# Kernel optimization log

Measured on AMD Instinct MI355X. Metric: run time of the kernel, lower is better.

Reference implementation:

```python
import jax, jax.numpy as jnp
import numpy as np

B, D_IN, H, D_OUT = 256, 512, 512, 10
S = 32          # num posterior samples
MAXITER = 10    # fixed CG steps (solve_normaleq_cg_fixed_step_reortho(maxiter=10))
EPS = 1e-12


def mlp(params, x):
    W1, b1, W2, b2 = params
    h = jnp.tanh(x @ W1 + b1)
    return h @ W2 + b2  # [B, D_OUT]


def setup_inputs() -> dict:
    key = jax.random.key(0)
    ks = jax.random.split(key, 8)
    s = lambda k, shape, scale=1.0: jax.random.normal(k, shape, dtype=jnp.float32) * scale
    return {
        "x": s(ks[0], (B, D_IN)),
        "W1": s(ks[1], (D_IN, H), 1.0 / np.sqrt(D_IN)),
        "b1": jnp.zeros((H,), jnp.float32),
        "W2": s(ks[2], (H, D_OUT), 1.0 / np.sqrt(H)),
        "b2": jnp.zeros((D_OUT,), jnp.float32),
        "eps_W1": s(ks[3], (S, D_IN, H)),
        "eps_b1": s(ks[4], (S, H)),
        "eps_W2": s(ks[5], (S, H, D_OUT)),
        "eps_b2": s(ks[6], (S, D_OUT)),
        "log_precision": jnp.zeros((), jnp.float32),
        "log_scale_image": jnp.asarray(-2.0, jnp.float32),
    }


def _posterior_predict(x, W1, b1, W2, b2, eps_W1, eps_b1, eps_W2, eps_b2,
                       log_precision, log_scale_image):
    params = (W1, b1, W2, b2)
    f = lambda p: mlp(p, x)
    out0, jvp_lin = jax.linearize(f, params)  # out0: [B, D_OUT]
    _, vjp_fn = jax.vjp(f, params)
    N = B * D_OUT

    def matvec(u_flat):  # u: [N] -> (J J^T) u : [N]
        (t,) = vjp_fn(u_flat.reshape(B, D_OUT))  # J^T u (param pytree)
        return jvp_lin(t).ravel()                # J J^T u

    def cg_reortho(b):  # fixed-step CG with full reorthogonalization
        rn0 = jnp.linalg.norm(b)
        basis0 = jnp.zeros((MAXITER + 1, N), b.dtype).at[0].set(b / (rn0 + EPS))

        def step(carry, k):
            a, r, p, basis = carry
            Ap = matvec(p)
            rr = jnp.vdot(r, r)
            alpha = rr / (jnp.vdot(p, Ap) + EPS)
            a = a + alpha * p
            r_new = r - alpha * Ap
            # Gram-Schmidt reorthogonalization against stored residual basis
            r_new = r_new - basis.T @ (basis @ r_new)
            beta = jnp.vdot(r_new, r_new) / (rr + EPS)
            p = r_new + beta * p
            basis = basis.at[k + 1].set(r_new / (jnp.linalg.norm(r_new) + EPS))
            return (a, r_new, p, basis), jnp.linalg.norm(r_new)

        init = (jnp.zeros_like(b), b, b, basis0)
        (a, _, _, _), resnorms = jax.lax.scan(step, init, jnp.arange(MAXITER))
        return a, resnorms

    def kernel_projection(eps):  # eps: param-pytree iso noise sample
        b = jvp_lin(eps).ravel()          # J v
        a, resnorms = cg_reortho(b)       # (J J^T)^{-1} J v
        (kv,) = vjp_fn(a.reshape(B, D_OUT))  # kernel component J^T a
        return kv, resnorms

    iso = (eps_W1, eps_b1, eps_W2, eps_b2)  # leading axis S
    kernel, resnorms = jax.vmap(kernel_projection)(iso)
    image = jax.tree_util.tree_map(lambda i, k: i - k, iso, kernel)

    # linearized output sampling: f(mean) + J @ (s_k * kernel + s_i * image)
    sk = jnp.exp(-0.5 * log_precision)  # log_scale_kernel = -0.5 * log_precision
    si = jnp.exp(log_scale_image)
    perturb = jax.tree_util.tree_map(lambda kv, iv: sk * kv + si * iv, kernel, image)
    preds = out0[None] + jax.vmap(jvp_lin)(perturb)  # [S, B, D_OUT]
    return preds


def reference(x, W1, b1, W2, b2, eps_W1, eps_b1, eps_W2, eps_b2,
              log_precision, log_scale_image):
    return _posterior_predict(x, W1, b1, W2, b2, eps_W1, eps_b1, eps_W2,
                              eps_b2, log_precision, log_scale_image)
```

## Files before the change

kernel.cpp:

```cpp
#include <hip/hip_runtime.h>
#include <math.h>

#define BB    256
#define DIN   512
#define HD    512
#define DOUT  10
#define NS    32
#define NIDX  2560
#define MAXIT 10
#define CG_EPS 1e-12f

typedef __attribute__((ext_vector_type(8))) short s16x8;
typedef __attribute__((ext_vector_type(4))) float f32x4;

__device__ __forceinline__ float wave_red(float v){
  #pragma unroll
  for (int off = 32; off > 0; off >>= 1) v += __shfl_down(v, off, 64);
  return v;
}
__device__ __forceinline__ unsigned short f2bf(float f){
  unsigned u = __float_as_uint(f);
  return (unsigned short)((u + 0x7FFFu + ((u >> 16) & 1u)) >> 16);
}
__device__ __forceinline__ float bf2f(unsigned short h){
  return __uint_as_float((unsigned)h << 16);
}

typedef const __attribute__((address_space(1))) unsigned short gus_t;
typedef __attribute__((address_space(3))) unsigned short lus_t;
__device__ __forceinline__ void gload16(const unsigned short* g, unsigned short* l){
  __builtin_amdgcn_global_load_lds((gus_t*)g, (lus_t*)l, 16, 0, 0);
}

__global__ __launch_bounds__(256) void k_gemm_z(
    const float* __restrict__ x, const float* __restrict__ W1,
    const float* __restrict__ b1, float* __restrict__ h, float* __restrict__ G)
{
  __shared__ __align__(16) float Al[16][68];
  __shared__ __align__(16) float Bl[16][64];
  const int tid = threadIdx.x;
  const int m0 = blockIdx.y * 64, n0 = blockIdx.x * 64;
  const int tx = tid & 15, ty = tid >> 4;
  float acc[4][4] = {};
  for (int k0 = 0; k0 < DIN; k0 += 16){
    {
      int m = tid >> 2, kk = (tid & 3) << 2;
      float4 a = *(const float4*)(x + (size_t)(m0+m)*DIN + k0 + kk);
      Al[kk+0][m]=a.x; Al[kk+1][m]=a.y; Al[kk+2][m]=a.z; Al[kk+3][m]=a.w;
    }
    {
      int kk = tid >> 4, n = (tid & 15) << 2;
      *(float4*)&Bl[kk][n] = *(const float4*)(W1 + (size_t)(k0+kk)*HD + n0 + n);
    }
    __syncthreads();
    #pragma unroll
    for (int kk = 0; kk < 16; kk++){
      float4 av = *(const float4*)&Al[kk][ty<<2];
      float4 bv = *(const float4*)&Bl[kk][tx<<2];
      float aa[4]={av.x,av.y,av.z,av.w}, bb[4]={bv.x,bv.y,bv.z,bv.w};
      #pragma unroll
      for (int i=0;i<4;i++)
        #pragma unroll
        for (int j=0;j<4;j++) acc[i][j] += aa[i]*bb[j];
    }
    __syncthreads();
  }
  float4 b4 = *(const float4*)&b1[n0 + (tx<<2)];
  float bbv[4] = {b4.x,b4.y,b4.z,b4.w};
  #pragma unroll
  for (int i=0;i<4;i++){
    int m = m0 + (ty<<2) + i;
    float hh[4], gg[4];
    #pragma unroll
    for (int j=0;j<4;j++){ float t = tanhf(acc[i][j] + bbv[j]); hh[j]=t; gg[j]=1.0f-t*t; }
    *(float4*)&h[(size_t)m*HD + n0 + (tx<<2)] = make_float4(hh[0],hh[1],hh[2],hh[3]);
    *(float4*)&G[(size_t)m*HD + n0 + (tx<<2)] = make_float4(gg[0],gg[1],gg[2],gg[3]);
  }
}

__global__ __launch_bounds__(256) void k_gemm_kxkh(
    const float* __restrict__ x, const float* __restrict__ h,
    float* __restrict__ Kx, float* __restrict__ Kh)
{
  __shared__ __align__(16) float Al[16][68];
  __shared__ __align__(16) float Bl[16][68];
  const int tid = threadIdx.x;
  const float* A = blockIdx.z ? h : x;
  float* C = blockIdx.z ? Kh : Kx;
  const int m0 = blockIdx.y * 64, n0 = blockIdx.x * 64;
  const int tx = tid & 15, ty = tid >> 4;
  float acc[4][4] = {};
  for (int k0 = 0; k0 < DIN; k0 += 16){
    {
      int m = tid >> 2, kk = (tid & 3) << 2;
      float4 a = *(const float4*)(A + (size_t)(m0+m)*DIN + k0 + kk);
      Al[kk+0][m]=a.x; Al[kk+1][m]=a.y; Al[kk+2][m]=a.z; Al[kk+3][m]=a.w;
      float4 b = *(const float4*)(A + (size_t)(n0+m)*DIN + k0 + kk);
      Bl[kk+0][m]=b.x; Bl[kk+1][m]=b.y; Bl[kk+2][m]=b.z; Bl[kk+3][m]=b.w;
    }
    __syncthreads();
    #pragma unroll
    for (int kk = 0; kk < 16; kk++){
      float4 av = *(const float4*)&Al[kk][ty<<2];
      float4 bv = *(const float4*)&Bl[kk][tx<<2];
      float aa[4]={av.x,av.y,av.z,av.w}, bb[4]={bv.x,bv.y,bv.z,bv.w};
      #pragma unroll
      for (int i=0;i<4;i++)
        #pragma unroll
        for (int j=0;j<4;j++) acc[i][j] += aa[i]*bb[j];
    }
    __syncthreads();
  }
  #pragma unroll
  for (int i=0;i<4;i++){
    int m = m0 + (ty<<2) + i;
    *(float4*)&C[(size_t)m*BB + n0 + (tx<<2)] =
        make_float4(acc[i][0]+1.0f, acc[i][1]+1.0f, acc[i][2]+1.0f, acc[i][3]+1.0f);
  }
}

__global__ __launch_bounds__(256) void k_buildE(
    const float* __restrict__ G, const float* __restrict__ W2,
    unsigned short* __restrict__ E2)
{
  int gid = blockIdx.x * 256 + threadIdx.x;
  int row = gid >> 7, j4 = (gid & 127) << 2;
  int b = row / 10, o = row - b * 10;
  float4 g = *(const float4*)&G[(size_t)b*HD + j4];
  float e[4] = { g.x * W2[(j4+0)*DOUT + o], g.y * W2[(j4+1)*DOUT + o],
                 g.z * W2[(j4+2)*DOUT + o], g.w * W2[(j4+3)*DOUT + o] };
  unsigned short hi[4], lo[4];
  #pragma unroll
  for (int r = 0; r < 4; r++){
    hi[r] = f2bf(e[r]);
    lo[r] = f2bf(e[r] - bf2f(hi[r]));
  }
  *(ushort4*)&E2[(size_t)row*1024 + j4]       = make_ushort4(hi[0],hi[1],hi[2],hi[3]);
  *(ushort4*)&E2[(size_t)row*1024 + 512 + j4] = make_ushort4(lo[0],lo[1],lo[2],lo[3]);
}

__global__ __launch_bounds__(256) void k_prepx(
    const float* __restrict__ x, unsigned short* __restrict__ x2)
{
  int gid = blockIdx.x * 256 + threadIdx.x;
  int row = gid >> 7, j4 = (gid & 127) << 2;
  float4 v = *(const float4*)&x[(size_t)row*DIN + j4];
  float e[4] = {v.x, v.y, v.z, v.w};
  unsigned short hi[4], lo[4];
  #pragma unroll
  for (int r = 0; r < 4; r++){
    hi[r] = f2bf(e[r]);
    lo[r] = f2bf(e[r] - bf2f(hi[r]));
  }
  *(ushort4*)&x2[(size_t)row*1024 + j4]       = make_ushort4(hi[0],hi[1],hi[2],hi[3]);
  *(ushort4*)&x2[(size_t)row*1024 + 512 + j4] = make_ushort4(lo[0],lo[1],lo[2],lo[3]);
}

__global__ __launch_bounds__(128) void k_gemm_M(
    const unsigned short* __restrict__ E2, const float* __restrict__ Kx,
    const float* __restrict__ Kh, unsigned short* __restrict__ M2)
{
  __shared__ __align__(16) unsigned short As[128*64];
  __shared__ __align__(16) unsigned short Bs[64*64];
  const int tid = threadIdx.x;
  const int w = tid >> 6, l = tid & 63;
  const int ln = l & 15, kq = l >> 4;
  const int orig = blockIdx.x;
  const int wg = (orig & 7) * 100 + (orig >> 3);
  const int m0 = (wg / 40) << 7, n0 = (wg % 40) << 6;

  const int srow = tid >> 3;
  const int scc  = (tid & 7) ^ (srow & 7);
  const unsigned short* gA = E2 + (size_t)(m0 + srow)*1024 + scc*8;
  const unsigned short* gB = E2 + (size_t)(n0 + srow)*1024 + scc*8;
  unsigned short* lA = As + ((tid & 64) << 3);
  unsigned short* lB = Bs + ((tid & 64) << 3);

  f32x4 acc[4][4];
  #pragma unroll
  for (int i = 0; i < 4; i++)
    #pragma unroll
    for (int j = 0; j < 4; j++)
      acc[i][j] = (f32x4){0.f, 0.f, 0.f, 0.f};

  const int xs = ln & 7;

  for (int t = 0; t < 24; ++t){
    const int p = t >> 3, k8 = t & 7;
    const int oa = ((p == 2) ? 512 : 0) + (k8 << 6);
    const int ob = ((p == 1) ? 512 : 0) + (k8 << 6);
    #pragma unroll
    for (int c = 0; c < 8; c++)
      gload16(gA + (size_t)c*16*1024 + oa, lA + c*1024);
    #pragma unroll
    for (int c = 0; c < 4; c++)
      gload16(gB + (size_t)c*16*1024 + ob, lB + c*1024);
    __syncthreads();

    #pragma unroll
    for (int kk = 0; kk < 2; kk++){
      const int kc = kq + (kk << 2);
      const int co = (kc ^ xs) << 3;
      s16x8 af[4], bf[4];
      #pragma unroll
      for (int f = 0; f < 4; f++){
        af[f] = *(const s16x8*)(As + ((w<<6) + (f<<4) + ln)*64 + co);
        bf[f] = *(const s16x8*)(Bs + ((f<<4) + ln)*64 + co);
      }
      #pragma unroll
      for (int fi = 0; fi < 4; fi++)
        #pragma unroll
        for (int fj = 0; fj < 4; fj++)
          acc[fi][fj] = __builtin_amdgcn_mfma_f32_16x16x32_bf16(
              af[fi], bf[fj], acc[fi][fj], 0, 0, 0);
    }
    __syncthreads();
  }

  const int mb = m0 + (w << 6);
  int bmv[4][4], omv[4][4], bnv[4], onv[4];
  #pragma unroll
  for (int f = 0; f < 4; f++){
    int n = n0 + f*16 + ln; bnv[f] = n / 10; onv[f] = n - bnv[f]*10;
    #pragma unroll
    for (int r = 0; r < 4; r++){
      int m = mb + f*16 + kq*4 + r;
      bmv[f][r] = m / 10; omv[f][r] = m - bmv[f][r]*10;
    }
  }
  #pragma unroll
  for (int fi = 0; fi < 4; fi++)
    #pragma unroll
    for (int r = 0; r < 4; r++){
      const int m = mb + fi*16 + kq*4 + r;
      #pragma unroll
      for (int fj = 0; fj < 4; fj++){
        const int n = n0 + fj*16 + ln;
        float v = Kx[(size_t)bmv[fi][r]*BB + bnv[fj]] * acc[fi][fj][r];
        if (omv[fi][r] == onv[fj]) v += Kh[(size_t)bmv[fi][r]*BB + bnv[fj]];
        unsigned short hv = f2bf(v);
        M2[(size_t)m*5120 + n]        = hv;
        M2[(size_t)m*5120 + 2560 + n] = f2bf(v - bf2f(hv));
      }
    }
}

__global__ __launch_bounds__(512) void k_gemm_T(
    const unsigned short* __restrict__ x2, const float* __restrict__ eW1,
    const float* __restrict__ eb1, const float* __restrict__ G,
    float* __restrict__ T)
{
  const int tid = threadIdx.x;
  const int w = tid >> 6, l = tid & 63;
  const int ln = l & 15, kq = l >> 4;
  const int n0 = blockIdx.x << 6;
  const int s  = blockIdx.y;
  const float* Wb = eW1 + (size_t)s * DIN * HD;

  const unsigned short* pa[2];
  #pragma unroll
  for (int f = 0; f < 2; f++)
    pa[f] = x2 + (size_t)(16*(2*w + f) + ln) * 1024 + kq * 8;

  f32x4 acc[2][4];
  #pragma unroll
  for (int i = 0; i < 2; i++)
    #pragma unroll
    for (int j = 0; j < 4; j++)
      acc[i][j] = (f32x4){0.f, 0.f, 0.f, 0.f};

  #pragma unroll 2
  for (int k0 = 0; k0 < DIN; k0 += 32){
    float wv[4][8];
    const float* wp = Wb + (size_t)(k0 + kq*8)*HD + n0 + ln;
    #pragma unroll
    for (int i = 0; i < 8; i++)
      #pragma unroll
      for (int f = 0; f < 4; f++)
        wv[f][i] = wp[(size_t)i*HD + 16*f];

    s16x8 ahi[2], alo[2], bhi[4], blo[4];
    #pragma unroll
    for (int f = 0; f < 2; f++){
      ahi[f] = *(const s16x8*)(pa[f] + k0);
      alo[f] = *(const s16x8*)(pa[f] + 512 + k0);
    }
    #pragma unroll
    for (int f = 0; f < 4; f++)
      #pragma unroll
      for (int i = 0; i < 8; i++){
        unsigned short hh = f2bf(wv[f][i]);
        bhi[f][i] = (short)hh;
        blo[f][i] = (short)f2bf(wv[f][i] - bf2f(hh));
      }
    #pragma unroll
    for (int fi = 0; fi < 2; fi++)
      #pragma unroll
      for (int fj = 0; fj < 4; fj++){
        acc[fi][fj] = __builtin_amdgcn_mfma_f32_16x16x32_bf16(ahi[fi], bhi[fj], acc[fi][fj], 0,0,0);
        acc[fi][fj] = __builtin_amdgcn_mfma_f32_16x16x32_bf16(ahi[fi], blo[fj], acc[fi][fj], 0,0,0);
        acc[fi][fj] = __builtin_amdgcn_mfma_f32_16x16x32_bf16(alo[fi], bhi[fj], acc[fi][fj], 0,0,0);
      }
  }

  #pragma unroll
  for (int fj = 0; fj < 4; fj++){
    const int n = n0 + 16*fj + ln;
    const float eb = eb1[(size_t)s*HD + n];
    #pragma unroll
    for (int fi = 0; fi < 2; fi++)
      #pragma unroll
      for (int q = 0; q < 4; q++){
        const int m = 16*(2*w + fi) + kq*4 + q;
        T[((size_t)s*BB + m)*HD + n] = (acc[fi][fj][q] + eb) * G[(size_t)m*HD + n];
      }
  }
}

__global__ __launch_bounds__(256) void k_bvec(
    const float* __restrict__ T, const float* __restrict__ W2,
    const float* __restrict__ h, const float* __restrict__ eW2,
    const float* __restrict__ eb2, const float* __restrict__ b2,
    float* __restrict__ bvec, float* __restrict__ out0, float* __restrict__ rr0_part)
{
  __shared__ __align__(16) float W2t[10][516];
  __shared__ __align__(16) float E2t[10][516];
  __shared__ float wl[4];
  const int tid = threadIdx.x, bid = blockIdx.x;
  const int s = bid / 10;
  const int idx = (bid % 10) * 256 + tid;
  const int b = idx / 10, o = idx - b*10;
  const float* e2 = eW2 + (size_t)s * HD * DOUT;
  for (int i = tid; i < HD*DOUT; i += 256){
    int k = i / 10, oo = i - k*10;
    W2t[oo][k] = W2[i];
    E2t[oo][k] = e2[i];
  }
  __syncthreads();
  const float* Tr = T + ((size_t)s*BB + b) * HD;
  const float* hr = h + (size_t)b * HD;
  const bool do0 = (bid < 10);
  float acc = eb2[s*DOUT + o];
  float a0 = 0.f;
  #pragma unroll 4
  for (int k4 = 0; k4 < HD/4; k4++){
    float4 t4 = *(const float4*)(Tr + (k4<<2));
    float4 h4 = *(const float4*)(hr + (k4<<2));
    float4 w4 = *(const float4*)&W2t[o][k4<<2];
    float4 q4 = *(const float4*)&E2t[o][k4<<2];
    acc += t4.x*w4.x + t4.y*w4.y + t4.z*w4.z + t4.w*w4.w
         + h4.x*q4.x + h4.y*q4.y + h4.z*q4.z + h4.w*q4.w;
    if (do0) a0 += h4.x*w4.x + h4.y*w4.y + h4.z*w4.z + h4.w*w4.w;
  }
  bvec[(size_t)s*NIDX + idx] = acc;
  if (do0) out0[idx] = a0 + b2[o];
  float v = wave_red(acc * acc);
  if ((tid & 63) == 0) wl[tid >> 6] = v;
  __syncthreads();
  if (tid == 0) rr0_part[bid] = wl[0]+wl[1]+wl[2]+wl[3];
}

__global__ __launch_bounds__(256) void k_init(
    const float* __restrict__ bvec, const float* __restrict__ rr0_part,
    float* __restrict__ r, float* __restrict__ p, float* __restrict__ a,
    float* __restrict__ basis, float* __restrict__ rr_arr,
    unsigned short* __restrict__ ps2)
{
  int gid = blockIdx.x * 256 + threadIdx.x;
  int s = gid / NIDX, idx = gid - s * NIDX;
  float rr0 = 0.f;
  #pragma unroll
  for (int i = 0; i < 10; i++) rr0 += rr0_part[s*10 + i];
  float bv = bvec[gid];
  r[gid] = bv; p[gid] = bv; a[gid] = 0.f;
  basis[gid] = bv / (sqrtf(rr0) + CG_EPS);
  unsigned short hh = f2bf(bv);
  ps2[(size_t)s*5120 + idx]        = hh;
  ps2[(size_t)s*5120 + 2560 + idx] = f2bf(bv - bf2f(hh));
  if (threadIdx.x == 0) rr_arr[s] = rr0;
}

__global__ __launch_bounds__(256) void k_matvec(
    const unsigned short* __restrict__ M2, const unsigned short* __restrict__ p2,
    float* __restrict__ Ap_part)
{
  __shared__ float red[4][16][33];
  const int tid = threadIdx.x;
  const int w = tid >> 6, l = tid & 63;
  const int ln = l & 15, kq = l >> 4;
  const int R0 = blockIdx.x << 4;
  const int kh = blockIdx.y;
  const int c0 = kh*640 + w*160;

  const unsigned short* a0p = M2 + (size_t)(R0 + ln)*5120 + c0 + kq*8;
  const unsigned short* q0  = p2 + (size_t)ln*5120        + c0 + kq*8;
  const unsigned short* q1  = p2 + (size_t)(16 + ln)*5120 + c0 + kq*8;

  f32x4 acc[2];
  acc[0] = (f32x4){0.f,0.f,0.f,0.f};
  acc[1] = (f32x4){0.f,0.f,0.f,0.f};

  #pragma unroll
  for (int ch = 0; ch < 5; ch++){
    const int o = ch * 32;
    s16x8 bh0 = *(const s16x8*)(q0 + o);
    s16x8 bl0 = *(const s16x8*)(q0 + 2560 + o);
    s16x8 bh1 = *(const s16x8*)(q1 + o);
    s16x8 bl1 = *(const s16x8*)(q1 + 2560 + o);
    s16x8 a0h = *(const s16x8*)(a0p + o);
    s16x8 a0l = *(const s16x8*)(a0p + 2560 + o);
    acc[0] = __builtin_amdgcn_mfma_f32_16x16x32_bf16(a0h, bh0, acc[0], 0,0,0);
    acc[1] = __builtin_amdgcn_mfma_f32_16x16x32_bf16(a0h, bh1, acc[1], 0,0,0);
    acc[0] = __builtin_amdgcn_mfma_f32_16x16x32_bf16(a0h, bl0, acc[0], 0,0,0);
    acc[1] = __builtin_amdgcn_mfma_f32_16x16x32_bf16(a0h, bl1, acc[1], 0,0,0);
    acc[0] = __builtin_amdgcn_mfma_f32_16x16x32_bf16(a0l, bh0, acc[0], 0,0,0);
    acc[1] = __builtin_amdgcn_mfma_f32_16x16x32_bf16(a0l, bh1, acc[1], 0,0,0);
  }

  #pragma unroll
  for (int g = 0; g < 2; g++)
    #pragma unroll
    for (int q = 0; q < 4; q++)
      red[w][kq*4 + q][16*g + ln] = acc[g][q];
  __syncthreads();
  #pragma unroll
  for (int j = 0; j < 2; j++){
    const int idx = tid + (j << 8);
    const int r = idx & 15, s = idx >> 4;
    float v = red[0][r][s] + red[1][r][s] + red[2][r][s] + red[3][r][s];
    Ap_part[((size_t)kh*NS + s)*NIDX + R0 + r] = v;
  }
}

__global__ __launch_bounds__(512) void k_cg(
    const float* __restrict__ Ap_part, float* __restrict__ rr_arr, int k, int last,
    float* __restrict__ pv, unsigned short* __restrict__ ps2,
    unsigned short* __restrict__ as2,
    float* __restrict__ av, float* __restrict__ rv, float* __restrict__ basis)
{
  __shared__ float wl[8];
  __shared__ float red[8][10];
  __shared__ float cbr[10];
  const int s = blockIdx.x, tid = threadIdx.x;
  const int w = tid >> 6;
  const size_t base = (size_t)s * NIDX;
  const float rr = rr_arr[s];

  float ap[5], pvv[5];
  #pragma unroll
  for (int c = 0; c < 5; c++){
    const int idx = tid + (c << 9);
    float apv = 0.f;
    #pragma unroll
    for (int kc = 0; kc < 4; kc++)
      apv += Ap_part[((size_t)kc*NS + s)*NIDX + idx];
    ap[c]  = apv;
    pvv[c] = pv[base + idx];
  }
  float v = 0.f;
  #pragma unroll
  for (int c = 0; c < 5; c++) v += pvv[c] * ap[c];
  v = wave_red(v);
  if ((tid & 63) == 0) wl[w] = v;
  __syncthreads();
  const float pAp = wl[0]+wl[1]+wl[2]+wl[3]+wl[4]+wl[5]+wl[6]+wl[7];
  const float alpha = rr / (pAp + CG_EPS);

  float rn[5];
  #pragma unroll
  for (int c = 0; c < 5; c++){
    const int idx = tid + (c << 9);
    const float an = av[base + idx] + alpha * pvv[c];
    av[base + idx] = an;
    rn[c] = rv[base + idx] - alpha * ap[c];
    if (last){
      unsigned short hh = f2bf(an);
      as2[(size_t)s*5120 + idx]        = hh;
      as2[(size_t)s*5120 + 2560 + idx] = f2bf(an - bf2f(hh));
    }
  }

  for (int j = 0; j <= k; j++){
    float cv = 0.f;
    const float* brow = basis + (size_t)j * (NS*NIDX) + base;
    #pragma unroll
    for (int c = 0; c < 5; c++) cv += brow[tid + (c << 9)] * rn[c];
    cv = wave_red(cv);
    if ((tid & 63) == 0) red[w][j] = cv;
  }
  __syncthreads();
  if (tid <= k){
    float cs = 0.f;
    #pragma unroll
    for (int ww = 0; ww < 8; ww++) cs += red[ww][tid];
    cbr[tid] = cs;
  }
  __syncthreads();

  for (int j = 0; j <= k; j++){
    const float cc = cbr[j];
    const float* brow = basis + (size_t)j * (NS*NIDX) + base;
    #pragma unroll
    for (int c = 0; c < 5; c++) rn[c] -= brow[tid + (c << 9)] * cc;
  }

  float rr2 = 0.f;
  #pragma unroll
  for (int c = 0; c < 5; c++) rr2 += rn[c]*rn[c];
  rr2 = wave_red(rr2);
  __syncthreads();
  if ((tid & 63) == 0) wl[w] = rr2;
  __syncthreads();
  const float rrn = wl[0]+wl[1]+wl[2]+wl[3]+wl[4]+wl[5]+wl[6]+wl[7];
  const float beta = rrn / (rr + CG_EPS);
  const float inv  = 1.0f / (sqrtf(rrn) + CG_EPS);

  float* bnew = basis + (size_t)(k+1) * (NS*NIDX) + base;
  #pragma unroll
  for (int c = 0; c < 5; c++){
    const int idx = tid + (c << 9);
    const float pnew = rn[c] + beta * pvv[c];
    rv[base + idx] = rn[c];
    pv[base + idx] = pnew;
    bnew[idx] = rn[c] * inv;
    unsigned short hh = f2bf(pnew);
    ps2[(size_t)s*5120 + idx]        = hh;
    ps2[(size_t)s*5120 + 2560 + idx] = f2bf(pnew - bf2f(hh));
  }
  if (tid == 0) rr_arr[s] = rrn;
}

__global__ __launch_bounds__(256) void k_final(
    const float* __restrict__ out0, const float* __restrict__ bvec,
    const float* __restrict__ Ap_part, const float* __restrict__ lp,
    const float* __restrict__ lsi, float* __restrict__ out)
{
  int gid = blockIdx.x * 256 + threadIdx.x;
  int s = gid / NIDX, idx = gid - s * NIDX;
  float sk = expf(-0.5f * lp[0]);
  float si = expf(lsi[0]);
  float ma = 0.f;
  #pragma unroll
  for (int kc = 0; kc < 4; kc++) ma += Ap_part[(size_t)kc*NS*NIDX + gid];
  out[gid] = out0[idx] + si * bvec[gid] + (sk - si) * ma;
}

extern "C" void kernel_launch(void* const* d_in, const int* in_sizes, int n_in,
                              void* d_out, int out_size, void* d_ws, size_t ws_size,
                              hipStream_t stream)
{
  const float* x   = (const float*)d_in[0];
  const float* W1  = (const float*)d_in[1];
  const float* b1  = (const float*)d_in[2];
  const float* W2  = (const float*)d_in[3];
  const float* b2  = (const float*)d_in[4];
  const float* eW1 = (const float*)d_in[5];
  const float* eb1 = (const float*)d_in[6];
  const float* eW2 = (const float*)d_in[7];
  const float* eb2 = (const float*)d_in[8];
  const float* lp  = (const float*)d_in[9];
  const float* lsi = (const float*)d_in[10];
  float* outp = (float*)d_out;

  float* ws = (float*)d_ws;
  float* h        = ws;
  float* G        = h        + 131072;
  float* Kx       = G        + 131072;
  float* Kh       = Kx       + 65536;
  float* E2f      = Kh       + 65536;
  float* x2f      = E2f      + 1310720;
  float* M2f      = x2f      + 131072;
  float* out0     = M2f      + 6553600;
  float* bvec     = out0     + 2560;
  float* rv       = bvec     + 81920;
  float* pv       = rv       + 81920;
  float* av       = pv       + 81920;
  float* basis    = av       + 81920;
  float* Ap_part  = basis    + 901120;
  float* ps2f     = Ap_part  + 327680;
  float* as2f     = ps2f     + 81920;
  float* rr0_part = as2f     + 81920;
  float* rr_arr   = rr0_part + 320;

  unsigned short* E2  = (unsigned short*)E2f;
  unsigned short* x2  = (unsigned short*)x2f;
  unsigned short* M2  = (unsigned short*)M2f;
  unsigned short* ps2 = (unsigned short*)ps2f;
  unsigned short* as2 = (unsigned short*)as2f;
  float* T = M2f;

  k_gemm_z   <<<dim3(8,4),   256, 0, stream>>>(x, W1, b1, h, G);
  k_buildE   <<<1280,        256, 0, stream>>>(G, W2, E2);
  k_prepx    <<<128,         256, 0, stream>>>(x, x2);
  k_gemm_kxkh<<<dim3(4,4,2), 256, 0, stream>>>(x, h, Kx, Kh);
  k_gemm_T   <<<dim3(8,32),  512, 0, stream>>>(x2, eW1, eb1, G, T);
  k_bvec     <<<320,         256, 0, stream>>>(T, W2, h, eW2, eb2, b2, bvec, out0, rr0_part);
  k_gemm_M   <<<800,         128, 0, stream>>>(E2, Kx, Kh, M2);
  k_init     <<<320,         256, 0, stream>>>(bvec, rr0_part, rv, pv, av, basis, rr_arr, ps2);

  for (int k = 0; k < MAXIT; k++){
    k_matvec<<<dim3(160,4), 256, 0, stream>>>(M2, ps2, Ap_part);
    k_cg    <<<NS,          512, 0, stream>>>(Ap_part, rr_arr, k, (k == MAXIT-1),
                                              pv, ps2, as2, av, rv, basis);
  }

  k_matvec<<<dim3(160,4), 256, 0, stream>>>(M2, as2, Ap_part);
  k_final <<<320,         256, 0, stream>>>(out0, bvec, Ap_part, lp, lsi, outp);
}
```

Before: 389.2 us.

## Merge prep kernels, retile gemm_M to 4 waves, use packed bf16 conversion

Merges the E2 and x2 split-precision prep kernels into one launch. Changes k_gemm_M from 2 waves with 64-row strips each to 4 waves with 32-row strips, a plain 2D grid, and no swizzled block order, which halves per-wave accumulators. Replaces the scalar bf16 hi/lo splitting in k_gemm_M and k_gemm_T with the packed v_cvt_pk_bf16_f32 instruction. The inline asm uses the hardware's rounding, which may differ slightly from the manual rounding, and dropping the block remap may change L2 locality.

```diff
diff --git a/kernel.cpp b/kernel.cpp
--- a/kernel.cpp
+++ b/kernel.cpp
@@ -12,6 +12,7 @@
 
 typedef __attribute__((ext_vector_type(8))) short s16x8;
 typedef __attribute__((ext_vector_type(4))) float f32x4;
+typedef __attribute__((ext_vector_type(4))) unsigned u32x4;
 
 __device__ __forceinline__ float wave_red(float v){
   #pragma unroll
@@ -24,6 +25,11 @@
 }
 __device__ __forceinline__ float bf2f(unsigned short h){
   return __uint_as_float((unsigned)h << 16);
+}
+__device__ __forceinline__ unsigned cvt_pk_bf16(float a, float b){
+  unsigned r;
+  asm("v_cvt_pk_bf16_f32 %0, %1, %2" : "=v"(r) : "v"(a), "v"(b));
+  return r;
 }
 
 typedef const __attribute__((address_space(1))) unsigned short gus_t;
@@ -119,44 +125,44 @@
   }
 }
 
-__global__ __launch_bounds__(256) void k_buildE(
+__global__ __launch_bounds__(256) void k_buildEx(
     const float* __restrict__ G, const float* __restrict__ W2,
-    unsigned short* __restrict__ E2)
-{
-  int gid = blockIdx.x * 256 + threadIdx.x;
-  int row = gid >> 7, j4 = (gid & 127) << 2;
-  int b = row / 10, o = row - b * 10;
-  float4 g = *(const float4*)&G[(size_t)b*HD + j4];
-  float e[4] = { g.x * W2[(j4+0)*DOUT + o], g.y * W2[(j4+1)*DOUT + o],
-                 g.z * W2[(j4+2)*DOUT + o], g.w * W2[(j4+3)*DOUT + o] };
-  unsigned short hi[4], lo[4];
-  #pragma unroll
-  for (int r = 0; r < 4; r++){
-    hi[r] = f2bf(e[r]);
-    lo[r] = f2bf(e[r] - bf2f(hi[r]));
-  }
-  *(ushort4*)&E2[(size_t)row*1024 + j4]       = make_ushort4(hi[0],hi[1],hi[2],hi[3]);
-  *(ushort4*)&E2[(size_t)row*1024 + 512 + j4] = make_ushort4(lo[0],lo[1],lo[2],lo[3]);
-}
-
-__global__ __launch_bounds__(256) void k_prepx(
-    const float* __restrict__ x, unsigned short* __restrict__ x2)
-{
-  int gid = blockIdx.x * 256 + threadIdx.x;
-  int row = gid >> 7, j4 = (gid & 127) << 2;
-  float4 v = *(const float4*)&x[(size_t)row*DIN + j4];
-  float e[4] = {v.x, v.y, v.z, v.w};
-  unsigned short hi[4], lo[4];
-  #pragma unroll
-  for (int r = 0; r < 4; r++){
-    hi[r] = f2bf(e[r]);
-    lo[r] = f2bf(e[r] - bf2f(hi[r]));
-  }
-  *(ushort4*)&x2[(size_t)row*1024 + j4]       = make_ushort4(hi[0],hi[1],hi[2],hi[3]);
-  *(ushort4*)&x2[(size_t)row*1024 + 512 + j4] = make_ushort4(lo[0],lo[1],lo[2],lo[3]);
-}
-
-__global__ __launch_bounds__(128) void k_gemm_M(
+    const float* __restrict__ x,
+    unsigned short* __restrict__ E2, unsigned short* __restrict__ x2)
+{
+  const int tid = threadIdx.x, bid = blockIdx.x;
+  if (bid < 1280){
+    int gid = bid * 256 + tid;
+    int row = gid >> 7, j4 = (gid & 127) << 2;
+    int b = row / 10, o = row - b * 10;
+    float4 g = *(const float4*)&G[(size_t)b*HD + j4];
+    float e[4] = { g.x * W2[(j4+0)*DOUT + o], g.y * W2[(j4+1)*DOUT + o],
+                   g.z * W2[(j4+2)*DOUT + o], g.w * W2[(j4+3)*DOUT + o] };
+    unsigned short hi[4], lo[4];
+    #pragma unroll
+    for (int r = 0; r < 4; r++){
+      hi[r] = f2bf(e[r]);
+      lo[r] = f2bf(e[r] - bf2f(hi[r]));
+    }
+    *(ushort4*)&E2[(size_t)row*1024 + j4]       = make_ushort4(hi[0],hi[1],hi[2],hi[3]);
+    *(ushort4*)&E2[(size_t)row*1024 + 512 + j4] = make_ushort4(lo[0],lo[1],lo[2],lo[3]);
+  } else {
+    int gid = (bid - 1280) * 256 + tid;
+    int row = gid >> 7, j4 = (gid & 127) << 2;
+    float4 v = *(const float4*)&x[(size_t)row*DIN + j4];
+    float e[4] = {v.x, v.y, v.z, v.w};
+    unsigned short hi[4], lo[4];
+    #pragma unroll
+    for (int r = 0; r < 4; r++){
+      hi[r] = f2bf(e[r]);
+      lo[r] = f2bf(e[r] - bf2f(hi[r]));
+    }
+    *(ushort4*)&x2[(size_t)row*1024 + j4]       = make_ushort4(hi[0],hi[1],hi[2],hi[3]);
+    *(ushort4*)&x2[(size_t)row*1024 + 512 + j4] = make_ushort4(lo[0],lo[1],lo[2],lo[3]);
+  }
+}
+
+__global__ __launch_bounds__(256) void k_gemm_M(
     const unsigned short* __restrict__ E2, const float* __restrict__ Kx,
     const float* __restrict__ Kh, unsigned short* __restrict__ M2)
 {
@@ -165,20 +171,18 @@
   const int tid = threadIdx.x;
   const int w = tid >> 6, l = tid & 63;
   const int ln = l & 15, kq = l >> 4;
-  const int orig = blockIdx.x;
-  const int wg = (orig & 7) * 100 + (orig >> 3);
-  const int m0 = (wg / 40) << 7, n0 = (wg % 40) << 6;
+  const int m0 = blockIdx.y << 7, n0 = blockIdx.x << 6;
 
   const int srow = tid >> 3;
   const int scc  = (tid & 7) ^ (srow & 7);
   const unsigned short* gA = E2 + (size_t)(m0 + srow)*1024 + scc*8;
   const unsigned short* gB = E2 + (size_t)(n0 + srow)*1024 + scc*8;
-  unsigned short* lA = As + ((tid & 64) << 3);
-  unsigned short* lB = Bs + ((tid & 64) << 3);
-
-  f32x4 acc[4][4];
-  #pragma unroll
-  for (int i = 0; i < 4; i++)
+  unsigned short* lA = As + w*512;
+  unsigned short* lB = Bs + w*512;
+
+  f32x4 acc[2][4];
+  #pragma unroll
+  for (int i = 0; i < 2; i++)
     #pragma unroll
     for (int j = 0; j < 4; j++)
       acc[i][j] = (f32x4){0.f, 0.f, 0.f, 0.f};
@@ -190,25 +194,26 @@
     const int oa = ((p == 2) ? 512 : 0) + (k8 << 6);
     const int ob = ((p == 1) ? 512 : 0) + (k8 << 6);
     #pragma unroll
-    for (int c = 0; c < 8; c++)
-      gload16(gA + (size_t)c*16*1024 + oa, lA + c*1024);
-    #pragma unroll
     for (int c = 0; c < 4; c++)
-      gload16(gB + (size_t)c*16*1024 + ob, lB + c*1024);
+      gload16(gA + (size_t)c*32*1024 + oa, lA + c*2048);
+    #pragma unroll
+    for (int c = 0; c < 2; c++)
+      gload16(gB + (size_t)c*32*1024 + ob, lB + c*2048);
     __syncthreads();
 
     #pragma unroll
     for (int kk = 0; kk < 2; kk++){
       const int kc = kq + (kk << 2);
       const int co = (kc ^ xs) << 3;
-      s16x8 af[4], bf[4];
-      #pragma unroll
-      for (int f = 0; f < 4; f++){
-        af[f] = *(const s16x8*)(As + ((w<<6) + (f<<4) + ln)*64 + co);
+      s16x8 af[2], bf[4];
+      #pragma unroll
+      for (int f = 0; f < 2; f++)
+        af[f] = *(const s16x8*)(As + ((w<<5) + (f<<4) + ln)*64 + co);
+      #pragma unroll
+      for (int f = 0; f < 4; f++)
         bf[f] = *(const s16x8*)(Bs + ((f<<4) + ln)*64 + co);
-      }
-      #pragma unroll
-      for (int fi = 0; fi < 4; fi++)
+      #pragma unroll
+      for (int fi = 0; fi < 2; fi++)
         #pragma unroll
         for (int fj = 0; fj < 4; fj++)
           acc[fi][fj] = __builtin_amdgcn_mfma_f32_16x16x32_bf16(
@@ -217,30 +222,43 @@
     __syncthreads();
   }
 
-  const int mb = m0 + (w << 6);
-  int bmv[4][4], omv[4][4], bnv[4], onv[4];
+  const int mb = m0 + (w << 5);
+  int bmv[2][4], omv[2][4], bnv[4], onv[4];
   #pragma unroll
   for (int f = 0; f < 4; f++){
     int n = n0 + f*16 + ln; bnv[f] = n / 10; onv[f] = n - bnv[f]*10;
+  }
+  #pragma unroll
+  for (int f = 0; f < 2; f++)
     #pragma unroll
     for (int r = 0; r < 4; r++){
       int m = mb + f*16 + kq*4 + r;
       bmv[f][r] = m / 10; omv[f][r] = m - bmv[f][r]*10;
     }
-  }
-  #pragma unroll
-  for (int fi = 0; fi < 4; fi++)
+  #pragma unroll
+  for (int fi = 0; fi < 2; fi++)
     #pragma unroll
     for (int r = 0; r < 4; r++){
       const int m = mb + fi*16 + kq*4 + r;
+      float v[4];
       #pragma unroll
       for (int fj = 0; fj < 4; fj++){
-        const int n = n0 + fj*16 + ln;
-        float v = Kx[(size_t)bmv[fi][r]*BB + bnv[fj]] * acc[fi][fj][r];
-        if (omv[fi][r] == onv[fj]) v += Kh[(size_t)bmv[fi][r]*BB + bnv[fj]];
-        unsigned short hv = f2bf(v);
-        M2[(size_t)m*5120 + n]        = hv;
-        M2[(size_t)m*5120 + 2560 + n] = f2bf(v - bf2f(hv));
+        float vv = Kx[(size_t)bmv[fi][r]*BB + bnv[fj]] * acc[fi][fj][r];
+        if (omv[fi][r] == onv[fj]) vv += Kh[(size_t)bmv[fi][r]*BB + bnv[fj]];
+        v[fj] = vv;
+      }
+      #pragma unroll
+      for (int p2 = 0; p2 < 2; p2++){
+        const float v0 = v[2*p2], v1 = v[2*p2+1];
+        const unsigned ph = cvt_pk_bf16(v0, v1);
+        const float h0 = __uint_as_float(ph << 16);
+        const float h1 = __uint_as_float(ph & 0xFFFF0000u);
+        const unsigned pl = cvt_pk_bf16(v0 - h0, v1 - h1);
+        const int na = n0 + (2*p2)*16 + ln, nb = na + 16;
+        M2[(size_t)m*5120 + na]        = (unsigned short)ph;
+        M2[(size_t)m*5120 + nb]        = (unsigned short)(ph >> 16);
+        M2[(size_t)m*5120 + 2560 + na] = (unsigned short)pl;
+        M2[(size_t)m*5120 + 2560 + nb] = (unsigned short)(pl >> 16);
       }
     }
 }
@@ -286,13 +304,20 @@
       alo[f] = *(const s16x8*)(pa[f] + 512 + k0);
     }
     #pragma unroll
-    for (int f = 0; f < 4; f++)
-      #pragma unroll
-      for (int i = 0; i < 8; i++){
-        unsigned short hh = f2bf(wv[f][i]);
-        bhi[f][i] = (short)hh;
-        blo[f][i] = (short)f2bf(wv[f][i] - bf2f(hh));
+    for (int f = 0; f < 4; f++){
+      u32x4 bh, bl;
+      #pragma unroll
+      for (int i = 0; i < 4; i++){
+        const float v0 = wv[f][2*i], v1 = wv[f][2*i+1];
+        const unsigned ph = cvt_pk_bf16(v0, v1);
+        bh[i] = ph;
+        const float h0 = __uint_as_float(ph << 16);
+        const float h1 = __uint_as_float(ph & 0xFFFF0000u);
+        bl[i] = cvt_pk_bf16(v0 - h0, v1 - h1);
       }
+      bhi[f] = __builtin_bit_cast(s16x8, bh);
+      blo[f] = __builtin_bit_cast(s16x8, bl);
+    }
     #pragma unroll
     for (int fi = 0; fi < 2; fi++)
       #pragma unroll
@@ -590,12 +615,11 @@
   float* T = M2f;
 
   k_gemm_z   <<<dim3(8,4),   256, 0, stream>>>(x, W1, b1, h, G);
-  k_buildE   <<<1280,        256, 0, stream>>>(G, W2, E2);
-  k_prepx    <<<128,         256, 0, stream>>>(x, x2);
+  k_buildEx  <<<1408,        256, 0, stream>>>(G, W2, x, E2, x2);
   k_gemm_kxkh<<<dim3(4,4,2), 256, 0, stream>>>(x, h, Kx, Kh);
   k_gemm_T   <<<dim3(8,32),  512, 0, stream>>>(x2, eW1, eb1, G, T);
   k_bvec     <<<320,         256, 0, stream>>>(T, W2, h, eW2, eb2, b2, bvec, out0, rr0_part);
-  k_gemm_M   <<<800,         128, 0, stream>>>(E2, Kx, Kh, M2);
+  k_gemm_M   <<<dim3(40,20), 256, 0, stream>>>(E2, Kx, Kh, M2);
   k_init     <<<320,         256, 0, stream>>>(bvec, rr0_part, rv, pv, av, basis, rr_arr, ps2);
 
   for (int k = 0; k < MAXIT; k++){
```

After: 374.4 us. -3.8%, faster.
